# Kernel tuning notes

Measured on AMD Instinct MI355X. Metric: run time of the kernel, lower is better.

## Reference

```python
import jax, jax.numpy as jnp
import numpy as np

B, S, D = 2, 2048, 768
H, STRIDE = 12, 8
HD = D // H  # 64


def setup_inputs() -> dict:
    key = jax.random.key(0)
    k0, k1, k2 = jax.random.split(key, 3)
    x = jax.random.normal(k0, (B, S, D), dtype=jnp.float32)
    qkv_w = jax.random.normal(k1, (3 * D, D), dtype=jnp.float32) * 0.02
    qkv_b = jnp.zeros((3 * D,), dtype=jnp.float32)
    out_w = jax.random.normal(k2, (D, D), dtype=jnp.float32) * 0.02
    out_b = jnp.zeros((D,), dtype=jnp.float32)
    return {"x": x, "qkv_w": qkv_w, "qkv_b": qkv_b, "out_w": out_w, "out_b": out_b}


def _stride_mask(S, stride, causal):
    i = jnp.arange(S)[:, None]
    j = jnp.arange(S)[None, :]
    strided = (j % stride == 0)
    if causal:
        strided = strided & (j <= i)
    # diagonal always attended; previous token attended for i > 0
    return strided | (j == i) | (j == i - 1)


def reference(x, qkv_w, qkv_b, out_w, out_b):
    Bx, Sx, Dx = x.shape
    qkv = x @ qkv_w.T + qkv_b                      # [B,S,3D]
    qkv = qkv.reshape(Bx, Sx, 3, H, HD)
    q, k, v = jnp.transpose(qkv, (2, 0, 3, 1, 4))  # each [B,H,S,HD]
    scale = HD ** -0.5
    attn = jnp.einsum('bhid,bhjd->bhij', q, k) * scale  # [B,H,S,S]
    mask = _stride_mask(Sx, STRIDE, True)          # [S,S] bool
    attn = jnp.where(mask[None, None], attn, -jnp.inf)
    a = jax.nn.softmax(attn, axis=-1)
    # every row has at least the diagonal unmasked, so no NaN rows;
    # nan_to_num kept for exact parity with the torch module
    a = jnp.nan_to_num(a, nan=0.0)
    out = jnp.einsum('bhij,bhjd->bhid', a, v)      # [B,H,S,HD]
    out = jnp.transpose(out, (0, 2, 1, 3)).reshape(Bx, Sx, Dx)
    return out @ out_w.T + out_b
```

## Files before the change

### kernel.cpp

```cpp
#include <hip/hip_runtime.h>
#include <hip/hip_bf16.h>
#include <stdint.h>

#define H_   12
#define S_   2048
#define D_   768
#define HD_  64
#define MS_  256

typedef __bf16 bf16_8 __attribute__((ext_vector_type(8)));
typedef float  f32_4  __attribute__((ext_vector_type(4)));

typedef __attribute__((address_space(1))) void* gas_ptr;
typedef __attribute__((address_space(3))) void* las_ptr;

__device__ __forceinline__ void g2l16(const void* g, void* l) {
  __builtin_amdgcn_global_load_lds((gas_ptr)g, (las_ptr)l, 16, 0, 0);
}

__device__ __forceinline__ f32_4 mfma16(bf16_8 a, bf16_8 b, f32_4 c) {
  return __builtin_amdgcn_mfma_f32_16x16x32_bf16(a, b, c, 0, 0, 0);
}

__device__ __forceinline__ bf16_8 ld8(const __hip_bfloat16* p) {
  return *reinterpret_cast<const bf16_8*>(p);
}

__global__ __launch_bounds__(256) void cvt_f32_bf16(
    const float* __restrict__ in, __hip_bfloat16* __restrict__ out, int n4) {
  const int t = blockIdx.x * 256 + threadIdx.x;
  if (t >= n4) return;
  const float4 f = reinterpret_cast<const float4*>(in)[t];
  union { __hip_bfloat16 h[4]; ushort4 u; } p;
  p.h[0] = __float2bfloat16(f.x);
  p.h[1] = __float2bfloat16(f.y);
  p.h[2] = __float2bfloat16(f.z);
  p.h[3] = __float2bfloat16(f.w);
  reinterpret_cast<ushort4*>(out)[t] = p.u;
}

template <int MODE>
__global__ __launch_bounds__(256, 2) void gemm_bt(
    const __hip_bfloat16* __restrict__ A, const __hip_bfloat16* __restrict__ B,
    const float* __restrict__ bias,
    __hip_bfloat16* __restrict__ O0, __hip_bfloat16* __restrict__ O1,
    __hip_bfloat16* __restrict__ O2, __hip_bfloat16* __restrict__ O3,
    float* __restrict__ OF, int M, int N, int K) {
  __shared__ __bf16 sA[128 * 32];
  __shared__ __bf16 sB[128 * 32];
  const int tid  = threadIdx.x;
  const int lane = tid & 63;
  const int wv   = tid >> 6;
  const int m0 = blockIdx.y * 128;
  const int n0 = blockIdx.x * 128;
  const int wr = (wv >> 1) * 64;
  const int wc = (wv & 1) * 64;

  f32_4 acc[4][4] = {};

  const __hip_bfloat16* aS = A + (size_t)(m0 + (tid >> 2)) * K + ((tid & 3) << 3);
  const __hip_bfloat16* bS = B + (size_t)(n0 + (tid >> 2)) * K + ((tid & 3) << 3);
  const size_t half = (size_t)64 * K;
  __bf16* dA  = &sA[tid * 8];
  __bf16* dA2 = &sA[tid * 8 + 2048];
  __bf16* dB  = &sB[tid * 8];
  __bf16* dB2 = &sB[tid * 8 + 2048];

  const int fr = lane & 15;
  const int kq = (lane >> 4) << 3;

  for (int k0 = 0; k0 < K; k0 += 32) {
    g2l16(aS, dA);
    g2l16(aS + half, dA2);
    g2l16(bS, dB);
    g2l16(bS + half, dB2);
    aS += 32;
    bS += 32;
    __syncthreads();
    bf16_8 af[4], bfm[4];
#pragma unroll
    for (int t = 0; t < 4; ++t)
      af[t] = *reinterpret_cast<const bf16_8*>(&sA[(wr + t * 16 + fr) * 32 + kq]);
#pragma unroll
    for (int t = 0; t < 4; ++t)
      bfm[t] = *reinterpret_cast<const bf16_8*>(&sB[(wc + t * 16 + fr) * 32 + kq]);
#pragma unroll
    for (int ti = 0; ti < 4; ++ti)
#pragma unroll
      for (int tj = 0; tj < 4; ++tj)
        acc[ti][tj] = mfma16(af[ti], bfm[tj], acc[ti][tj]);
    __syncthreads();
  }

  const int crow = (lane >> 4) << 2;
  const int ccol = lane & 15;
#pragma unroll
  for (int ti = 0; ti < 4; ++ti) {
    const int gmb = m0 + wr + ti * 16 + crow;
#pragma unroll
    for (int tj = 0; tj < 4; ++tj) {
      const int gn = n0 + wc + tj * 16 + ccol;
      const float bv = bias[gn];
      if (MODE == 0) {
        const int t   = gn / D_;
        const int rem = gn - t * D_;
        const int hh = rem >> 6, dd = rem & 63;
        if (t < 2) {
          __hip_bfloat16* dst = (t == 0) ? O0 : O1;
#pragma unroll
          for (int r = 0; r < 4; ++r) {
            const int gm = gmb + r;
            const int bb = gm >> 11, ss = gm & (S_ - 1);
            dst[(((size_t)(bb * H_ + hh) << 11) + ss) * HD_ + dd] =
                __float2bfloat16(acc[ti][tj][r] + bv);
          }
        } else {
          const int bb = gmb >> 11, ss = gmb & (S_ - 1);
          union { ushort4 u; __hip_bfloat16 h[4]; } pk;
#pragma unroll
          for (int r = 0; r < 4; ++r) pk.h[r] = __float2bfloat16(acc[ti][tj][r] + bv);
          const size_t rowb = ((size_t)(bb * H_ + hh) * HD_ + dd);
          *reinterpret_cast<ushort4*>(O2 + rowb * S_ + ss) = pk.u;
          if ((ss & 7) == 0) O3[rowb * MS_ + (ss >> 3)] = pk.h[0];
        }
      } else {
#pragma unroll
        for (int r = 0; r < 4; ++r)
          OF[(size_t)(gmb + r) * D_ + gn] = acc[ti][tj][r] + bv;
      }
    }
  }
}

__global__ __launch_bounds__(256) void attn_mfma(
    const __hip_bfloat16* __restrict__ Q, const __hip_bfloat16* __restrict__ Kb,
    const __hip_bfloat16* __restrict__ VT, const __hip_bfloat16* __restrict__ VsT,
    __hip_bfloat16* __restrict__ ctx) {
  __shared__ __bf16 pt[4][16 * 40];
  const int lane = threadIdx.x & 63;
  const int wv   = threadIdx.x >> 6;
  const int task = blockIdx.x * 4 + wv;
  const int bh   = task >> 7;
  const int i0   = (task & 127) << 4;
  const int lr   = lane & 15;
  const int quad = lane >> 4;
  const float SC  = 0.125f * 1.44269504088896340736f;
  const float NEG = -1e30f;

  const __hip_bfloat16* Kh  = Kb  + ((size_t)bh << 11) * HD_;
  const __hip_bfloat16* VTh = VT  + (size_t)bh * HD_ * S_;
  const __hip_bfloat16* Vsh = VsT + (size_t)bh * HD_ * MS_;
  __bf16* ptw = pt[wv];

  const __hip_bfloat16* qp = Q + (((size_t)bh << 11) + i0 + lr) * HD_ + quad * 8;
  const bf16_8 qf0 = ld8(qp);
  const bf16_8 qf1 = ld8(qp + 32);

  f32_4 M, L, oacc[4];
#pragma unroll
  for (int r = 0; r < 4; ++r) { M[r] = NEG; L[r] = 0.f; }
#pragma unroll
  for (int ct = 0; ct < 4; ++ct) oacc[ct] = f32_4{0.f, 0.f, 0.f, 0.f};

  const int mmax = (i0 + 15) >> 3;
  const int nstr = (mmax >> 5) + 1;
  for (int c = 0; c <= nstr; ++c) {
    const bool strided = (c < nstr);
    const int  mb    = c << 5;
    const int  jbase = (i0 >= 8) ? (i0 - 8) : 0;

    bf16_8 kf[2][2], vf[4];
    if (strided) {
#pragma unroll
      for (int t = 0; t < 2; ++t) {
        const int m = mb + t * 16 + lr;
        const __hip_bfloat16* kp = Kh + ((size_t)m << 3) * HD_ + quad * 8;
        kf[t][0] = ld8(kp);
        kf[t][1] = ld8(kp + 32);
      }
#pragma unroll
      for (int ct = 0; ct < 4; ++ct)
        vf[ct] = ld8(Vsh + (size_t)(ct * 16 + lr) * MS_ + mb + quad * 8);
    } else {
#pragma unroll
      for (int t = 0; t < 2; ++t) {
        const int j  = jbase + t * 16 + lr;
        const int jr = (j < S_) ? j : (S_ - 1);
        const __hip_bfloat16* kp = Kh + (size_t)jr * HD_ + quad * 8;
        kf[t][0] = ld8(kp);
        kf[t][1] = ld8(kp + 32);
      }
      const int vs0 = jbase + quad * 8;
      const int vs  = (vs0 <= S_ - 8) ? vs0 : (S_ - 8);
#pragma unroll
      for (int ct = 0; ct < 4; ++ct)
        vf[ct] = ld8(VTh + (size_t)(ct * 16 + lr) * S_ + vs);
    }

    f32_4 s0 = {}, s1 = {};
    s0 = mfma16(qf0, kf[0][0], s0);
    s0 = mfma16(qf1, kf[0][1], s0);
    s1 = mfma16(qf0, kf[1][0], s1);
    s1 = mfma16(qf1, kf[1][1], s1);

#pragma unroll
    for (int r = 0; r < 4; ++r) {
      const int i = i0 + quad * 4 + r;
      bool v0, v1;
      if (strided) {
        v0 = ((mb + lr) << 3) <= i;
        v1 = ((mb + 16 + lr) << 3) <= i;
      } else {
        const int j0 = jbase + lr, j1 = jbase + 16 + lr;
        v0 = (j0 == i || j0 == i - 1) && (j0 & 7);
        v1 = (j1 == i || j1 == i - 1) && (j1 & 7);
      }
      s0[r] = v0 ? s0[r] * SC : NEG;
      s1[r] = v1 ? s1[r] * SC : NEG;
    }

    f32_4 mx;
#pragma unroll
    for (int r = 0; r < 4; ++r) mx[r] = fmaxf(s0[r], s1[r]);
#pragma unroll
    for (int d = 1; d < 16; d <<= 1)
#pragma unroll
      for (int r = 0; r < 4; ++r) mx[r] = fmaxf(mx[r], __shfl_xor(mx[r], d));

    f32_4 p0, p1, alpha, rs;
#pragma unroll
    for (int r = 0; r < 4; ++r) {
      const float Mn = fmaxf(M[r], mx[r]);
      p0[r]    = exp2f(s0[r] - Mn);
      p1[r]    = exp2f(s1[r] - Mn);
      alpha[r] = exp2f(M[r] - Mn);
      M[r]     = Mn;
      rs[r]    = p0[r] + p1[r];
    }
#pragma unroll
    for (int d = 1; d < 16; d <<= 1)
#pragma unroll
      for (int r = 0; r < 4; ++r) rs[r] += __shfl_xor(rs[r], d);
#pragma unroll
    for (int r = 0; r < 4; ++r) L[r] = L[r] * alpha[r] + rs[r];
#pragma unroll
    for (int ct = 0; ct < 4; ++ct)
#pragma unroll
      for (int r = 0; r < 4; ++r) oacc[ct][r] *= alpha[r];

#pragma unroll
    for (int r = 0; r < 4; ++r) {
      const int row = quad * 4 + r;
      ptw[row * 40 + lr]      = (__bf16)__float2bfloat16(p0[r]);
      ptw[row * 40 + 16 + lr] = (__bf16)__float2bfloat16(p1[r]);
    }
    const bf16_8 pf = *reinterpret_cast<const bf16_8*>(&ptw[lr * 40 + quad * 8]);

#pragma unroll
    for (int ct = 0; ct < 4; ++ct) oacc[ct] = mfma16(pf, vf[ct], oacc[ct]);
  }

  const int b = bh / H_;
  const int h = bh - b * H_;
  f32_4 inv;
#pragma unroll
  for (int r = 0; r < 4; ++r) inv[r] = 1.f / L[r];
#pragma unroll
  for (int r = 0; r < 4; ++r) {
    const int i = i0 + quad * 4 + r;
    __hip_bfloat16* cp = ctx + ((size_t)(b * S_ + i)) * D_ + h * HD_ + lr;
#pragma unroll
    for (int ct = 0; ct < 4; ++ct)
      cp[ct * 16] = __float2bfloat16(oacc[ct][r] * inv[r]);
  }
}

extern "C" void kernel_launch(void* const* d_in, const int* in_sizes, int n_in,
                              void* d_out, int out_size, void* d_ws, size_t ws_size,
                              hipStream_t stream) {
  const float* x    = (const float*)d_in[0];
  const float* qkvw = (const float*)d_in[1];
  const float* qkvb = (const float*)d_in[2];
  const float* outw = (const float*)d_in[3];
  const float* outb = (const float*)d_in[4];
  float* out = (float*)d_out;

  const size_t NX  = (size_t)2 * S_ * D_;
  const size_t NW1 = (size_t)3 * D_ * D_;
  const size_t NW2 = (size_t)D_ * D_;
  const size_t NVS = (size_t)2 * H_ * HD_ * MS_;

  __hip_bfloat16* xb  = (__hip_bfloat16*)d_ws;
  __hip_bfloat16* w1b = xb + NX;
  __hip_bfloat16* w2b = w1b + NW1;
  __hip_bfloat16* q   = w2b + NW2;
  __hip_bfloat16* k   = q + NX;
  __hip_bfloat16* vt  = k + NX;
  __hip_bfloat16* vst = vt + NX;
  __hip_bfloat16* ctx = vst + NVS;

  cvt_f32_bf16<<<dim3((int)(NX  / 4 / 256)), 256, 0, stream>>>(x,    xb,  (int)(NX  / 4));
  cvt_f32_bf16<<<dim3((int)(NW1 / 4 / 256)), 256, 0, stream>>>(qkvw, w1b, (int)(NW1 / 4));
  cvt_f32_bf16<<<dim3((int)(NW2 / 4 / 256)), 256, 0, stream>>>(outw, w2b, (int)(NW2 / 4));

  gemm_bt<0><<<dim3(2304 / 128, 4096 / 128), 256, 0, stream>>>(
      xb, w1b, qkvb, q, k, vt, vst, nullptr, 4096, 2304, 768);

  attn_mfma<<<dim3(2 * H_ * S_ / 16 / 4), 256, 0, stream>>>(q, k, vt, vst, ctx);

  gemm_bt<1><<<dim3(768 / 128, 4096 / 128), 256, 0, stream>>>(
      ctx, w2b, outb, nullptr, nullptr, nullptr, nullptr, out, 4096, 768, 768);
}
```

Before: 157.9 us.

## Drop online-softmax max tracking and fuse the three f32-to-bf16 conversions

```diff
diff --git a/kernel.cpp b/kernel.cpp
--- a/kernel.cpp
+++ b/kernel.cpp
@@ -26,11 +26,15 @@
   return *reinterpret_cast<const bf16_8*>(p);
 }
 
-__global__ __launch_bounds__(256) void cvt_f32_bf16(
-    const float* __restrict__ in, __hip_bfloat16* __restrict__ out, int n4) {
+__global__ __launch_bounds__(256) void cvt3_f32_bf16(
+    const float* __restrict__ a, const float* __restrict__ b,
+    const float* __restrict__ c, __hip_bfloat16* __restrict__ out,
+    int na4, int nb4) {
   const int t = blockIdx.x * 256 + threadIdx.x;
-  if (t >= n4) return;
-  const float4 f = reinterpret_cast<const float4*>(in)[t];
+  float4 f;
+  if (t < na4)            f = reinterpret_cast<const float4*>(a)[t];
+  else if (t < na4 + nb4) f = reinterpret_cast<const float4*>(b)[t - na4];
+  else                    f = reinterpret_cast<const float4*>(c)[t - na4 - nb4];
   union { __hip_bfloat16 h[4]; ushort4 u; } p;
   p.h[0] = __float2bfloat16(f.x);
   p.h[1] = __float2bfloat16(f.y);
@@ -145,7 +149,6 @@
   const int lr   = lane & 15;
   const int quad = lane >> 4;
   const float SC  = 0.125f * 1.44269504088896340736f;
-  const float NEG = -1e30f;
 
   const __hip_bfloat16* Kh  = Kb  + ((size_t)bh << 11) * HD_;
   const __hip_bfloat16* VTh = VT  + (size_t)bh * HD_ * S_;
@@ -156,9 +159,10 @@
   const bf16_8 qf0 = ld8(qp);
   const bf16_8 qf1 = ld8(qp + 32);
 
-  f32_4 M, L, oacc[4];
-#pragma unroll
-  for (int r = 0; r < 4; ++r) { M[r] = NEG; L[r] = 0.f; }
+  const __bf16 one = (__bf16)1.0f;
+  const bf16_8 onesf = {one, one, one, one, one, one, one, one};
+
+  f32_4 Lacc = {}, oacc[4];
 #pragma unroll
   for (int ct = 0; ct < 4; ++ct) oacc[ct] = f32_4{0.f, 0.f, 0.f, 0.f};
 
@@ -215,56 +219,28 @@
         v0 = (j0 == i || j0 == i - 1) && (j0 & 7);
         v1 = (j1 == i || j1 == i - 1) && (j1 & 7);
       }
-      s0[r] = v0 ? s0[r] * SC : NEG;
-      s1[r] = v1 ? s1[r] * SC : NEG;
-    }
-
-    f32_4 mx;
-#pragma unroll
-    for (int r = 0; r < 4; ++r) mx[r] = fmaxf(s0[r], s1[r]);
-#pragma unroll
-    for (int d = 1; d < 16; d <<= 1)
-#pragma unroll
-      for (int r = 0; r < 4; ++r) mx[r] = fmaxf(mx[r], __shfl_xor(mx[r], d));
-
-    f32_4 p0, p1, alpha, rs;
-#pragma unroll
-    for (int r = 0; r < 4; ++r) {
-      const float Mn = fmaxf(M[r], mx[r]);
-      p0[r]    = exp2f(s0[r] - Mn);
-      p1[r]    = exp2f(s1[r] - Mn);
-      alpha[r] = exp2f(M[r] - Mn);
-      M[r]     = Mn;
-      rs[r]    = p0[r] + p1[r];
-    }
-#pragma unroll
-    for (int d = 1; d < 16; d <<= 1)
-#pragma unroll
-      for (int r = 0; r < 4; ++r) rs[r] += __shfl_xor(rs[r], d);
-#pragma unroll
-    for (int r = 0; r < 4; ++r) L[r] = L[r] * alpha[r] + rs[r];
-#pragma unroll
-    for (int ct = 0; ct < 4; ++ct)
-#pragma unroll
-      for (int r = 0; r < 4; ++r) oacc[ct][r] *= alpha[r];
+      s0[r] = v0 ? exp2f(fminf(s0[r] * SC, 63.f)) : 0.f;
+      s1[r] = v1 ? exp2f(fminf(s1[r] * SC, 63.f)) : 0.f;
+    }
 
 #pragma unroll
     for (int r = 0; r < 4; ++r) {
       const int row = quad * 4 + r;
-      ptw[row * 40 + lr]      = (__bf16)__float2bfloat16(p0[r]);
-      ptw[row * 40 + 16 + lr] = (__bf16)__float2bfloat16(p1[r]);
+      ptw[row * 40 + lr]      = (__bf16)__float2bfloat16(s0[r]);
+      ptw[row * 40 + 16 + lr] = (__bf16)__float2bfloat16(s1[r]);
     }
     const bf16_8 pf = *reinterpret_cast<const bf16_8*>(&ptw[lr * 40 + quad * 8]);
 
 #pragma unroll
     for (int ct = 0; ct < 4; ++ct) oacc[ct] = mfma16(pf, vf[ct], oacc[ct]);
+    Lacc = mfma16(pf, onesf, Lacc);
   }
 
   const int b = bh / H_;
   const int h = bh - b * H_;
   f32_4 inv;
 #pragma unroll
-  for (int r = 0; r < 4; ++r) inv[r] = 1.f / L[r];
+  for (int r = 0; r < 4; ++r) inv[r] = 1.f / Lacc[r];
 #pragma unroll
   for (int r = 0; r < 4; ++r) {
     const int i = i0 + quad * 4 + r;
@@ -299,9 +275,9 @@
   __hip_bfloat16* vst = vt + NX;
   __hip_bfloat16* ctx = vst + NVS;
 
-  cvt_f32_bf16<<<dim3((int)(NX  / 4 / 256)), 256, 0, stream>>>(x,    xb,  (int)(NX  / 4));
-  cvt_f32_bf16<<<dim3((int)(NW1 / 4 / 256)), 256, 0, stream>>>(qkvw, w1b, (int)(NW1 / 4));
-  cvt_f32_bf16<<<dim3((int)(NW2 / 4 / 256)), 256, 0, stream>>>(outw, w2b, (int)(NW2 / 4));
+  const int na4 = (int)(NX / 4), nb4 = (int)(NW1 / 4), nc4 = (int)(NW2 / 4);
+  cvt3_f32_bf16<<<dim3((na4 + nb4 + nc4) / 256), 256, 0, stream>>>(
+      x, qkvw, outw, xb, na4, nb4);
 
   gemm_bt<0><<<dim3(2304 / 128, 4096 / 128), 256, 0, stream>>>(
       xb, w1b, qkvb, q, k, vt, vst, nullptr, 4096, 2304, 768);
```

Result: faster. 154.2 us (-2.3%).
